# Kernel tuning notes

Hardware: AMD Instinct MI355X
Metric: run time of the kernel (lower is better)

Reference implementation:

```python
import jax, jax.numpy as jnp
import numpy as np

M = 12          # persons per frame
K = 2           # partition channels from conv1da (1024 = 2*512)
D = 512         # GCN channel dim / LSTM hidden
C_IN = 4096     # backbone feature dim
NUM_CLASSES = 8


def setup_inputs() -> dict:
    key = jax.random.key(0)
    ks = jax.random.split(key, 8)
    N, T = 16, 32
    NT = N * T
    base_out = jax.random.normal(ks[0], (NT, M, C_IN), dtype=jnp.float32)
    dist = jax.random.uniform(ks[1], (N, T, 3, K, M, M), dtype=jnp.float32)
    # conv1da: Conv1d(4096 -> 1024, k=1, bias=False) == matmul with [1024, 4096]
    w_a = jax.random.normal(ks[2], (K * D, C_IN), dtype=jnp.float32) * 0.02
    # LSTM(512, 512, 1): torch gate order i, f, g, o
    s = 1.0 / np.sqrt(D)
    w_ih = jax.random.uniform(ks[3], (4 * D, D), minval=-s, maxval=s, dtype=jnp.float32)
    w_hh = jax.random.uniform(ks[4], (4 * D, D), minval=-s, maxval=s, dtype=jnp.float32)
    b_ih = jax.random.uniform(ks[5], (4 * D,), minval=-s, maxval=s, dtype=jnp.float32)
    b_hh = jax.random.uniform(ks[6], (4 * D,), minval=-s, maxval=s, dtype=jnp.float32)
    # gclassifier: Linear(512 -> num_classes)
    w_cls = jax.random.normal(ks[7], (NUM_CLASSES, D), dtype=jnp.float32) * 0.01
    b_cls = jnp.zeros((NUM_CLASSES,), dtype=jnp.float32)
    return {"base_out": base_out, "dist": dist, "w_a": w_a,
            "w_ih": w_ih, "w_hh": w_hh, "b_ih": b_ih, "b_hh": b_hh,
            "w_cls": w_cls, "b_cls": b_cls, "n_videos": N}


def reference(base_out, dist, w_a, w_ih, w_hh, b_ih, b_hh, w_cls, b_cls, n_videos):
    NT = base_out.shape[0]
    N = n_videos
    T = NT // N
    # conv1da (1x1 conv, no bias): [NT, M, 4096] -> [NT, K*D, M] -> [NT, K, D, M]
    node1 = jnp.einsum('nmc,oc->nom', base_out, w_a).reshape(NT, K, D, M)
    # fused three-way adjacency aggregation: node1a + node1b + node1c
    A = (dist[:, :, 2] + dist[:, :, 1] + dist[:, :, 0]).reshape(NT, K, M, M)
    node = jnp.einsum('nkcv,nkvw->ncw', node1, A)  # [NT, D, M]
    node = jax.nn.relu(node)
    # AdaptiveAvgPool1d(1) over the M persons
    pooled = node.mean(axis=2)                      # [NT, D]
    seq = pooled.reshape(N, T, D)
    # torch nn.LSTM default batch_first=False: iterates over axis 0 (N), batch=T
    def step(carry, x_t):
        h, c = carry
        g = x_t @ w_ih.T + b_ih + h @ w_hh.T + b_hh  # [T, 4D]
        i, f, gg, o = jnp.split(g, 4, axis=-1)
        c = jax.nn.sigmoid(f) * c + jax.nn.sigmoid(i) * jnp.tanh(gg)
        h = jax.nn.sigmoid(o) * jnp.tanh(c)
        return (h, c), h
    h0 = jnp.zeros((T, D), dtype=seq.dtype)
    c0 = jnp.zeros((T, D), dtype=seq.dtype)
    _, hs = jax.lax.scan(step, (h0, c0), seq)       # [N, T, D]
    last = hs[:, -1, :]                              # video_feat[:, -1, :]
    return last @ w_cls.T + b_cls                    # [N, num_classes]
```

## Files before the change

kernel.cpp:

```cpp
#include <hip/hip_runtime.h>
#include <math.h>

#define MM 12
#define KK 2
#define DD 512
#define CIN 4096
#define NCLS 8
#define NV 16
#define TT 32

typedef unsigned long long u64;

#define PART_F   0
#define POOLED_F 786432
#define GX_F     794624
#define SLOT_F   827392

__global__ __launch_bounds__(256) void k_gemm(const float* __restrict__ w_a,
                                              const float* __restrict__ base_out,
                                              float* __restrict__ part) {
    const int ks = blockIdx.x;
    const int ot = blockIdx.y;
    const int jt = blockIdx.z;
    const int tid = threadIdx.x;

    __shared__ __align__(16) float As[16][68];
    __shared__ __align__(16) float Bs[16][52];

    const int to = tid & 15;
    const int tj = tid >> 4;

    const int arow = tid >> 2;
    const int aq   = tid & 3;
    const size_t a_base = (size_t)(ot * 64 + arow) * CIN;

    const int brow = tid >> 2;
    const int j_stage = jt * 48 + brow;
    const int n_stage = j_stage / 12;
    const int m_stage = j_stage - n_stage * 12;
    const size_t b_base = (size_t)((n_stage * TT + 31) * MM + m_stage) * CIN;

    float acc[4][3];
#pragma unroll
    for (int i = 0; i < 4; ++i)
#pragma unroll
        for (int jj = 0; jj < 3; ++jj) acc[i][jj] = 0.f;

    int cc0 = ks * 1024;
    float4 av = *(const float4*)&w_a[a_base + cc0 + aq * 4];
    float4 bv;
    if (tid < 192) bv = *(const float4*)&base_out[b_base + cc0 + aq * 4];

    for (int it = 0; it < 64; ++it) {
        __syncthreads();
        As[aq * 4 + 0][arow] = av.x; As[aq * 4 + 1][arow] = av.y;
        As[aq * 4 + 2][arow] = av.z; As[aq * 4 + 3][arow] = av.w;
        if (tid < 192) {
            Bs[aq * 4 + 0][brow] = bv.x; Bs[aq * 4 + 1][brow] = bv.y;
            Bs[aq * 4 + 2][brow] = bv.z; Bs[aq * 4 + 3][brow] = bv.w;
        }
        __syncthreads();
        if (it < 63) {
            cc0 += 16;
            av = *(const float4*)&w_a[a_base + cc0 + aq * 4];
            if (tid < 192) bv = *(const float4*)&base_out[b_base + cc0 + aq * 4];
        }
#pragma unroll
        for (int cl = 0; cl < 16; ++cl) {
            float4 a = *(const float4*)&As[cl][to * 4];
            float b0 = Bs[cl][tj];
            float b1 = Bs[cl][tj + 16];
            float b2 = Bs[cl][tj + 32];
            acc[0][0] += a.x * b0; acc[0][1] += a.x * b1; acc[0][2] += a.x * b2;
            acc[1][0] += a.y * b0; acc[1][1] += a.y * b1; acc[1][2] += a.y * b2;
            acc[2][0] += a.z * b0; acc[2][1] += a.z * b1; acc[2][2] += a.z * b2;
            acc[3][0] += a.w * b0; acc[3][1] += a.w * b1; acc[3][2] += a.w * b2;
        }
    }

    const int o_base = ot * 64 + to * 4;
#pragma unroll
    for (int jj = 0; jj < 3; ++jj) {
        const int j = jt * 48 + tj + 16 * jj;
        float4 v = make_float4(acc[0][jj], acc[1][jj], acc[2][jj], acc[3][jj]);
        *(float4*)&part[(size_t)ks * (192 * 1024) + (size_t)j * 1024 + o_base] = v;
    }
}

__global__ __launch_bounds__(256) void k_pool(const float* __restrict__ part,
                                              const float* __restrict__ dist,
                                              float* __restrict__ pooled) {
    const int n = blockIdx.x;
    const int tid = threadIdx.x;
    __shared__ float Asum[KK][MM][MM];

    const size_t dbase = (size_t)(n * TT + 31) * (3 * KK * MM * MM);
    for (int f = tid; f < KK * MM * MM; f += 256) {
        const int k = f / (MM * MM);
        const int rem = f - k * (MM * MM);
        float s = dist[dbase + 0 * (KK * MM * MM) + k * (MM * MM) + rem]
                + dist[dbase + 1 * (KK * MM * MM) + k * (MM * MM) + rem]
                + dist[dbase + 2 * (KK * MM * MM) + k * (MM * MM) + rem];
        Asum[k][rem / MM][rem % MM] = s;
    }
    __syncthreads();

    for (int c = tid; c < DD; c += 256) {
        float nd[KK][MM];
#pragma unroll
        for (int k = 0; k < KK; ++k)
#pragma unroll
            for (int v = 0; v < MM; ++v) {
                const size_t off = (size_t)(n * MM + v) * 1024 + (k * DD + c);
                nd[k][v] = part[off] + part[off + 1 * (192 * 1024)]
                         + part[off + 2 * (192 * 1024)] + part[off + 3 * (192 * 1024)];
            }
        float accm = 0.f;
#pragma unroll
        for (int w = 0; w < MM; ++w) {
            float sw = 0.f;
#pragma unroll
            for (int k = 0; k < KK; ++k)
#pragma unroll
                for (int v = 0; v < MM; ++v) sw += nd[k][v] * Asum[k][v][w];
            accm += fmaxf(sw, 0.f);
        }
        pooled[n * DD + c] = accm * (1.f / 12.f);
    }
}

__global__ __launch_bounds__(256) void k_gx(const float* __restrict__ pooled,
                                            const float* __restrict__ w_ih,
                                            const float* __restrict__ b_ih,
                                            const float* __restrict__ b_hh,
                                            float* __restrict__ gx) {
    const int wg = blockIdx.x;
    const int tid = threadIdx.x;
    __shared__ __align__(16) float w_s[16][516];

    for (int f = tid; f < 16 * DD; f += 256) {
        const int r = f >> 9, col = f & 511;
        w_s[r][col] = w_ih[(size_t)(wg * 16 + r) * DD + col];
    }
    __syncthreads();

    const int r = tid & 15;
    const int n = tid >> 4;
    const float4* wr = (const float4*)&w_s[r][0];
    const float4* pv = (const float4*)(pooled + n * DD);
    float acc = 0.f;
#pragma unroll 8
    for (int q = 0; q < DD / 4; ++q) {
        float4 a = wr[q], b = pv[q];
        acc += a.x * b.x + a.y * b.y + a.z * b.z + a.w * b.w;
    }
    const int row = wg * 16 + r;
    gx[n * (4 * DD) + row] = acc + b_ih[row] + b_hh[row];
}

__global__ __launch_bounds__(256) void k_lstm(const float* __restrict__ w_hh,
                                              const float* __restrict__ gx,
                                              const float* __restrict__ w_cls,
                                              const float* __restrict__ b_cls,
                                              u64* __restrict__ slots,
                                              float* __restrict__ out) {
    const int wg = blockIdx.x;
    const int tid = threadIdx.x;

    __shared__ __align__(16) float whh_s[64][516];
    __shared__ __align__(16) float h_s[DD];
    __shared__ float dot_s[64];

    for (int f = tid; f < 64 * 128; f += 256) {
        const int rl = f >> 7, q = f & 127;
        const int gate = rl >> 4, dl = rl & 15;
        float4 v = *(const float4*)&w_hh[(size_t)(gate * DD + wg * 16 + dl) * DD + q * 4];
        *(float4*)&whh_s[rl][q * 4] = v;
    }

    float c_reg = 0.f;
    const int r  = tid >> 2;
    const int lp = tid & 3;

    for (int s = 0; s < NV; ++s) {
        if (s == 0) {
            for (int d = tid; d < DD; d += 256) h_s[d] = 0.f;
        } else {
            const u64* slot = slots + (size_t)(s - 1) * DD;
            for (int d = tid; d < DD; d += 256) {
                u64 v = __hip_atomic_load(&slot[d], __ATOMIC_RELAXED, __HIP_MEMORY_SCOPE_AGENT);
                while ((unsigned)(v & 0xffffffffull) != (unsigned)s) {
                    __builtin_amdgcn_s_sleep(1);
                    v = __hip_atomic_load(&slot[d], __ATOMIC_RELAXED, __HIP_MEMORY_SCOPE_AGENT);
                }
                union { unsigned u; float f; } cv; cv.u = (unsigned)(v >> 32);
                h_s[d] = cv.f;
            }
        }
        __syncthreads();

        float p = 0.f;
        const float4* wrow = (const float4*)&whh_s[r][0];
        const float4* hv4 = (const float4*)h_s;
#pragma unroll
        for (int q = 0; q < 32; ++q) {
            float4 wv = wrow[lp + 4 * q];
            float4 hv = hv4[lp + 4 * q];
            p += wv.x * hv.x + wv.y * hv.y + wv.z * hv.z + wv.w * hv.w;
        }
        p += __shfl_down(p, 2, 4);
        p += __shfl_down(p, 1, 4);
        if (lp == 0) dot_s[r] = p;
        __syncthreads();

        if (tid < 16) {
            const int dg = wg * 16 + tid;
            const float* gxs = gx + s * (4 * DD);
            const float pi = gxs[0 * DD + dg] + dot_s[0  + tid];
            const float pf = gxs[1 * DD + dg] + dot_s[16 + tid];
            const float pg = gxs[2 * DD + dg] + dot_s[32 + tid];
            const float po = gxs[3 * DD + dg] + dot_s[48 + tid];
            const float si = 1.f / (1.f + expf(-pi));
            const float sf = 1.f / (1.f + expf(-pf));
            const float so = 1.f / (1.f + expf(-po));
            c_reg = sf * c_reg + si * tanhf(pg);
            const float hn = so * tanhf(c_reg);
            union { float f; unsigned u; } hv_; hv_.f = hn;
            const u64 pack = ((u64)hv_.u << 32) | (u64)(unsigned)(s + 1);
            __hip_atomic_store(&slots[(size_t)s * DD + dg], pack,
                               __ATOMIC_RELAXED, __HIP_MEMORY_SCOPE_AGENT);
        }
    }

    if (wg == 0) {
        for (int f = tid; f < NV * DD; f += 256) {
            const int ss = f >> 9, d = f & 511;
            u64 v = __hip_atomic_load(&slots[(size_t)ss * DD + d],
                                      __ATOMIC_RELAXED, __HIP_MEMORY_SCOPE_AGENT);
            while ((unsigned)(v & 0xffffffffull) != (unsigned)(ss + 1)) {
                __builtin_amdgcn_s_sleep(1);
                v = __hip_atomic_load(&slots[(size_t)ss * DD + d],
                                      __ATOMIC_RELAXED, __HIP_MEMORY_SCOPE_AGENT);
            }
            union { unsigned u; float f; } cv; cv.u = (unsigned)(v >> 32);
            whh_s[ss][d] = cv.f;
        }
        __syncthreads();
        if (tid < NV * NCLS) {
            const int n = tid >> 3, cl = tid & 7;
            const float4* hv = (const float4*)&whh_s[n][0];
            const float4* wv = (const float4*)(w_cls + (size_t)cl * DD);
            float acc = b_cls[cl];
#pragma unroll 8
            for (int q = 0; q < DD / 4; ++q) {
                float4 a = hv[q], b = wv[q];
                acc += a.x * b.x + a.y * b.y + a.z * b.z + a.w * b.w;
            }
            out[tid] = acc;
        }
    }
}

extern "C" void kernel_launch(void* const* d_in, const int* in_sizes, int n_in,
                              void* d_out, int out_size, void* d_ws, size_t ws_size,
                              hipStream_t stream) {
    const float* base_out = (const float*)d_in[0];
    const float* dist     = (const float*)d_in[1];
    const float* w_a      = (const float*)d_in[2];
    const float* w_ih     = (const float*)d_in[3];
    const float* w_hh     = (const float*)d_in[4];
    const float* b_ih     = (const float*)d_in[5];
    const float* b_hh     = (const float*)d_in[6];
    const float* w_cls    = (const float*)d_in[7];
    const float* b_cls    = (const float*)d_in[8];
    float* out = (float*)d_out;

    float* ws = (float*)d_ws;
    float* part   = ws + PART_F;
    float* pooled = ws + POOLED_F;
    float* gx     = ws + GX_F;
    u64*   slots  = (u64*)(ws + SLOT_F);

    k_gemm<<<dim3(4, 16, 4), 256, 0, stream>>>(w_a, base_out, part);
    k_pool<<<dim3(16), 256, 0, stream>>>(part, dist, pooled);
    k_gx<<<dim3(128), 256, 0, stream>>>(pooled, w_ih, b_ih, b_hh, gx);
    k_lstm<<<dim3(32), 256, 0, stream>>>(w_hh, gx, w_cls, b_cls, slots, out);
}
```

Baseline: 292.0 us.

## Widen GEMM tiles, raise split-K, and spread LSTM over more workgroups

The GEMM now has each block cover all 192 needed rows with 4x12 register tiles, and split-K goes from 4 to 16 when the workspace is big enough. The pool kernel sums a variable number of partials. The LSTM recurrence is spread over 128 workgroups of 512 threads, each owning 4 hidden units, with one thread per slot polling without sleep. The aim is more parallelism on the GEMM and a shorter per-step dot product in the serial LSTM. The cost is extra partial-sum traffic and more cross-workgroup spin polling.

```diff
diff --git a/kernel.cpp b/kernel.cpp
--- a/kernel.cpp
+++ b/kernel.cpp
@@ -11,21 +11,24 @@
 
 typedef unsigned long long u64;
 
-#define PART_F   0
-#define POOLED_F 786432
-#define GX_F     794624
-#define SLOT_F   827392
-
+#define POOLED_F 0
+#define GX_F     8192
+#define SLOT_F   40960
+#define PART_F   57344
+#define PART_STRIDE (192 * 1024)
+
+template <int KS>
 __global__ __launch_bounds__(256) void k_gemm(const float* __restrict__ w_a,
                                               const float* __restrict__ base_out,
                                               float* __restrict__ part) {
     const int ks = blockIdx.x;
     const int ot = blockIdx.y;
-    const int jt = blockIdx.z;
     const int tid = threadIdx.x;
+    constexpr int CHUNK = CIN / KS;
+    constexpr int ITS = CHUNK / 16;
 
     __shared__ __align__(16) float As[16][68];
-    __shared__ __align__(16) float Bs[16][52];
+    __shared__ __align__(16) float Bs[16][196];
 
     const int to = tid & 15;
     const int tj = tid >> 4;
@@ -34,62 +37,75 @@
     const int aq   = tid & 3;
     const size_t a_base = (size_t)(ot * 64 + arow) * CIN;
 
-    const int brow = tid >> 2;
-    const int j_stage = jt * 48 + brow;
-    const int n_stage = j_stage / 12;
-    const int m_stage = j_stage - n_stage * 12;
-    const size_t b_base = (size_t)((n_stage * TT + 31) * MM + m_stage) * CIN;
-
-    float acc[4][3];
+    size_t b_base[3];
+#pragma unroll
+    for (int rep = 0; rep < 3; ++rep) {
+        const int j = arow + 64 * rep;
+        const int n = j / 12, m = j - n * 12;
+        b_base[rep] = (size_t)((n * TT + 31) * MM + m) * CIN;
+    }
+
+    float acc[4][12];
 #pragma unroll
     for (int i = 0; i < 4; ++i)
 #pragma unroll
-        for (int jj = 0; jj < 3; ++jj) acc[i][jj] = 0.f;
-
-    int cc0 = ks * 1024;
+        for (int jj = 0; jj < 12; ++jj) acc[i][jj] = 0.f;
+
+    int cc0 = ks * CHUNK;
     float4 av = *(const float4*)&w_a[a_base + cc0 + aq * 4];
-    float4 bv;
-    if (tid < 192) bv = *(const float4*)&base_out[b_base + cc0 + aq * 4];
-
-    for (int it = 0; it < 64; ++it) {
+    float4 bv[3];
+#pragma unroll
+    for (int rep = 0; rep < 3; ++rep)
+        bv[rep] = *(const float4*)&base_out[b_base[rep] + cc0 + aq * 4];
+
+    for (int it = 0; it < ITS; ++it) {
         __syncthreads();
         As[aq * 4 + 0][arow] = av.x; As[aq * 4 + 1][arow] = av.y;
         As[aq * 4 + 2][arow] = av.z; As[aq * 4 + 3][arow] = av.w;
-        if (tid < 192) {
-            Bs[aq * 4 + 0][brow] = bv.x; Bs[aq * 4 + 1][brow] = bv.y;
-            Bs[aq * 4 + 2][brow] = bv.z; Bs[aq * 4 + 3][brow] = bv.w;
-        }
-        __syncthreads();
-        if (it < 63) {
+#pragma unroll
+        for (int rep = 0; rep < 3; ++rep) {
+            const int br = arow + 64 * rep;
+            Bs[aq * 4 + 0][br] = bv[rep].x; Bs[aq * 4 + 1][br] = bv[rep].y;
+            Bs[aq * 4 + 2][br] = bv[rep].z; Bs[aq * 4 + 3][br] = bv[rep].w;
+        }
+        __syncthreads();
+        if (it < ITS - 1) {
             cc0 += 16;
             av = *(const float4*)&w_a[a_base + cc0 + aq * 4];
-            if (tid < 192) bv = *(const float4*)&base_out[b_base + cc0 + aq * 4];
+#pragma unroll
+            for (int rep = 0; rep < 3; ++rep)
+                bv[rep] = *(const float4*)&base_out[b_base[rep] + cc0 + aq * 4];
         }
 #pragma unroll
         for (int cl = 0; cl < 16; ++cl) {
-            float4 a = *(const float4*)&As[cl][to * 4];
-            float b0 = Bs[cl][tj];
-            float b1 = Bs[cl][tj + 16];
-            float b2 = Bs[cl][tj + 32];
-            acc[0][0] += a.x * b0; acc[0][1] += a.x * b1; acc[0][2] += a.x * b2;
-            acc[1][0] += a.y * b0; acc[1][1] += a.y * b1; acc[1][2] += a.y * b2;
-            acc[2][0] += a.z * b0; acc[2][1] += a.z * b1; acc[2][2] += a.z * b2;
-            acc[3][0] += a.w * b0; acc[3][1] += a.w * b1; acc[3][2] += a.w * b2;
+            float4 a  = *(const float4*)&As[cl][to * 4];
+            float4 b0 = *(const float4*)&Bs[cl][tj * 12 + 0];
+            float4 b1 = *(const float4*)&Bs[cl][tj * 12 + 4];
+            float4 b2 = *(const float4*)&Bs[cl][tj * 12 + 8];
+            const float bb[12] = {b0.x,b0.y,b0.z,b0.w, b1.x,b1.y,b1.z,b1.w,
+                                  b2.x,b2.y,b2.z,b2.w};
+#pragma unroll
+            for (int jj = 0; jj < 12; ++jj) {
+                acc[0][jj] += a.x * bb[jj];
+                acc[1][jj] += a.y * bb[jj];
+                acc[2][jj] += a.z * bb[jj];
+                acc[3][jj] += a.w * bb[jj];
+            }
         }
     }
 
     const int o_base = ot * 64 + to * 4;
 #pragma unroll
-    for (int jj = 0; jj < 3; ++jj) {
-        const int j = jt * 48 + tj + 16 * jj;
+    for (int jj = 0; jj < 12; ++jj) {
+        const int j = tj * 12 + jj;
         float4 v = make_float4(acc[0][jj], acc[1][jj], acc[2][jj], acc[3][jj]);
-        *(float4*)&part[(size_t)ks * (192 * 1024) + (size_t)j * 1024 + o_base] = v;
+        *(float4*)&part[(size_t)ks * PART_STRIDE + (size_t)j * 1024 + o_base] = v;
     }
 }
 
 __global__ __launch_bounds__(256) void k_pool(const float* __restrict__ part,
                                               const float* __restrict__ dist,
-                                              float* __restrict__ pooled) {
+                                              float* __restrict__ pooled, int KS) {
     const int n = blockIdx.x;
     const int tid = threadIdx.x;
     __shared__ float Asum[KK][MM][MM];
@@ -112,8 +128,10 @@
 #pragma unroll
             for (int v = 0; v < MM; ++v) {
                 const size_t off = (size_t)(n * MM + v) * 1024 + (k * DD + c);
-                nd[k][v] = part[off] + part[off + 1 * (192 * 1024)]
-                         + part[off + 2 * (192 * 1024)] + part[off + 3 * (192 * 1024)];
+                float s = 0.f;
+                for (int ks = 0; ks < KS; ++ks)
+                    s += part[off + (size_t)ks * PART_STRIDE];
+                nd[k][v] = s;
             }
         float accm = 0.f;
 #pragma unroll
@@ -158,7 +176,7 @@
     gx[n * (4 * DD) + row] = acc + b_ih[row] + b_hh[row];
 }
 
-__global__ __launch_bounds__(256) void k_lstm(const float* __restrict__ w_hh,
+__global__ __launch_bounds__(512) void k_lstm(const float* __restrict__ w_hh,
                                               const float* __restrict__ gx,
                                               const float* __restrict__ w_cls,
                                               const float* __restrict__ b_cls,
@@ -167,35 +185,31 @@
     const int wg = blockIdx.x;
     const int tid = threadIdx.x;
 
-    __shared__ __align__(16) float whh_s[64][516];
+    __shared__ __align__(16) float whh_s[16][516];
     __shared__ __align__(16) float h_s[DD];
-    __shared__ float dot_s[64];
-
-    for (int f = tid; f < 64 * 128; f += 256) {
-        const int rl = f >> 7, q = f & 127;
-        const int gate = rl >> 4, dl = rl & 15;
-        float4 v = *(const float4*)&w_hh[(size_t)(gate * DD + wg * 16 + dl) * DD + q * 4];
-        *(float4*)&whh_s[rl][q * 4] = v;
+    __shared__ float dot_s[16];
+
+    for (int f = tid; f < 16 * DD; f += 512) {
+        const int rl = f >> 9, col = f & 511;
+        const int gate = rl >> 2, dl = rl & 3;
+        whh_s[rl][col] = w_hh[(size_t)(gate * DD + wg * 4 + dl) * DD + col];
     }
 
     float c_reg = 0.f;
-    const int r  = tid >> 2;
-    const int lp = tid & 3;
+    const int r  = tid >> 5;
+    const int lp = tid & 31;
 
     for (int s = 0; s < NV; ++s) {
         if (s == 0) {
-            for (int d = tid; d < DD; d += 256) h_s[d] = 0.f;
+            h_s[tid < DD ? tid : 0] = 0.f;
         } else {
             const u64* slot = slots + (size_t)(s - 1) * DD;
-            for (int d = tid; d < DD; d += 256) {
-                u64 v = __hip_atomic_load(&slot[d], __ATOMIC_RELAXED, __HIP_MEMORY_SCOPE_AGENT);
-                while ((unsigned)(v & 0xffffffffull) != (unsigned)s) {
-                    __builtin_amdgcn_s_sleep(1);
-                    v = __hip_atomic_load(&slot[d], __ATOMIC_RELAXED, __HIP_MEMORY_SCOPE_AGENT);
-                }
-                union { unsigned u; float f; } cv; cv.u = (unsigned)(v >> 32);
-                h_s[d] = cv.f;
-            }
+            u64 v = __hip_atomic_load(&slot[tid], __ATOMIC_RELAXED, __HIP_MEMORY_SCOPE_AGENT);
+            while ((unsigned)(v & 0xffffffffull) != (unsigned)s) {
+                v = __hip_atomic_load(&slot[tid], __ATOMIC_RELAXED, __HIP_MEMORY_SCOPE_AGENT);
+            }
+            union { unsigned u; float f; } cv; cv.u = (unsigned)(v >> 32);
+            h_s[tid] = cv.f;
         }
         __syncthreads();
 
@@ -203,23 +217,23 @@
         const float4* wrow = (const float4*)&whh_s[r][0];
         const float4* hv4 = (const float4*)h_s;
 #pragma unroll
-        for (int q = 0; q < 32; ++q) {
-            float4 wv = wrow[lp + 4 * q];
-            float4 hv = hv4[lp + 4 * q];
+        for (int q = 0; q < 4; ++q) {
+            float4 wv = wrow[lp + 32 * q];
+            float4 hv = hv4[lp + 32 * q];
             p += wv.x * hv.x + wv.y * hv.y + wv.z * hv.z + wv.w * hv.w;
         }
-        p += __shfl_down(p, 2, 4);
-        p += __shfl_down(p, 1, 4);
+#pragma unroll
+        for (int off = 16; off; off >>= 1) p += __shfl_down(p, off, 32);
         if (lp == 0) dot_s[r] = p;
         __syncthreads();
 
-        if (tid < 16) {
-            const int dg = wg * 16 + tid;
+        if (tid < 4) {
+            const int dg = wg * 4 + tid;
             const float* gxs = gx + s * (4 * DD);
             const float pi = gxs[0 * DD + dg] + dot_s[0  + tid];
-            const float pf = gxs[1 * DD + dg] + dot_s[16 + tid];
-            const float pg = gxs[2 * DD + dg] + dot_s[32 + tid];
-            const float po = gxs[3 * DD + dg] + dot_s[48 + tid];
+            const float pf = gxs[1 * DD + dg] + dot_s[4  + tid];
+            const float pg = gxs[2 * DD + dg] + dot_s[8  + tid];
+            const float po = gxs[3 * DD + dg] + dot_s[12 + tid];
             const float si = 1.f / (1.f + expf(-pi));
             const float sf = 1.f / (1.f + expf(-pf));
             const float so = 1.f / (1.f + expf(-po));
@@ -233,12 +247,11 @@
     }
 
     if (wg == 0) {
-        for (int f = tid; f < NV * DD; f += 256) {
+        for (int f = tid; f < NV * DD; f += 512) {
             const int ss = f >> 9, d = f & 511;
             u64 v = __hip_atomic_load(&slots[(size_t)ss * DD + d],
                                       __ATOMIC_RELAXED, __HIP_MEMORY_SCOPE_AGENT);
             while ((unsigned)(v & 0xffffffffull) != (unsigned)(ss + 1)) {
-                __builtin_amdgcn_s_sleep(1);
                 v = __hip_atomic_load(&slots[(size_t)ss * DD + d],
                                       __ATOMIC_RELAXED, __HIP_MEMORY_SCOPE_AGENT);
             }
@@ -276,13 +289,17 @@
     float* out = (float*)d_out;
 
     float* ws = (float*)d_ws;
-    float* part   = ws + PART_F;
     float* pooled = ws + POOLED_F;
     float* gx     = ws + GX_F;
     u64*   slots  = (u64*)(ws + SLOT_F);
-
-    k_gemm<<<dim3(4, 16, 4), 256, 0, stream>>>(w_a, base_out, part);
-    k_pool<<<dim3(16), 256, 0, stream>>>(part, dist, pooled);
+    float* part   = ws + PART_F;
+
+    const size_t need16 = ((size_t)PART_F + (size_t)16 * PART_STRIDE) * 4;
+    const bool big = ws_size >= need16;
+
+    if (big) k_gemm<16><<<dim3(16, 16), 256, 0, stream>>>(w_a, base_out, part);
+    else     k_gemm<4> <<<dim3(4, 16),  256, 0, stream>>>(w_a, base_out, part);
+    k_pool<<<dim3(16), 256, 0, stream>>>(part, dist, pooled, big ? 16 : 4);
     k_gx<<<dim3(128), 256, 0, stream>>>(pooled, w_ih, b_ih, b_hh, gx);
-    k_lstm<<<dim3(32), 256, 0, stream>>>(w_hh, gx, w_cls, b_cls, slots, out);
-}
+    k_lstm<<<dim3(128), 512, 0, stream>>>(w_hh, gx, w_cls, b_cls, slots, out);
+}
```

Result: slower. 428.4 us (+46.7%).
